# Kernel tuning notes

Measured on AMD Instinct MI355X. Metric: run time of the kernel, lower is better.

Reference implementation:

```python
import jax, jax.numpy as jnp
import numpy as np

B, M, N = 1, 8192, 131072      # batch, bones, window points
C_BOT, C = 16, 128             # bottleneck_channel, channel
K_MAX, FOLD, R_UP = 8, 8, 4    # max neighbors, fold_channel, upsample rate r
EPS = 1e-8


def _lin_init(key, fan_in, fan_out):
    return jax.random.normal(key, (fan_in, fan_out), jnp.float32) / np.sqrt(fan_in)


def setup_inputs() -> dict:
    key = jax.random.key(0)
    ks = jax.random.split(key, 10)
    return {
        "quantized_cf": jax.random.normal(ks[0], (B, M, C_BOT), jnp.float32),
        "d_idx": jax.random.randint(ks[1], (B, N, K_MAX), 0, M),
        "d_windows": jax.random.normal(ks[2], (B, N, 3), jnp.float32),
        "bones": jax.random.normal(ks[3], (B, M, 3), jnp.float32),
        "K": 8,
        # fea_stretch Linear(bottleneck -> channel)
        "W_stretch": _lin_init(ks[4], C_BOT, C),
        "b_stretch": jnp.zeros((C,), jnp.float32),
        # DWUS folding MLP: (C+3) -> C -> FOLD*R_UP -> 3 (per fold point)
        "W1": _lin_init(ks[5], C + 3, C),
        "b1": jnp.zeros((C,), jnp.float32),
        "W2": _lin_init(ks[6], C, FOLD * R_UP),
        "b2": jnp.zeros((FOLD * R_UP,), jnp.float32),
        "W3": _lin_init(ks[7], FOLD, 3),
        "b3": jnp.zeros((3,), jnp.float32),
    }


def reference(quantized_cf, d_idx, d_windows, bones, K,
              W_stretch, b_stretch, W1, b1, W2, b2, W3, b3):
    # fea_stretch: per-bone feature expansion  [B, M, C]
    skin_fea = jnp.einsum("bmc,cd->bmd", quantized_cf, W_stretch) + b_stretch

    idx = d_idx[..., :K]                                   # [B, N, K]
    batch = jnp.arange(B)[:, None, None]
    g_fea = skin_fea[batch, idx]                           # [B, N, K, C] gather
    g_bones = bones[batch, idx]                            # [B, N, K, 3]

    # inverse-distance interpolation of bone features onto window points
    rel = d_windows[:, :, None, :] - g_bones               # [B, N, K, 3]
    dist = jnp.sqrt(jnp.sum(rel * rel, axis=-1) + EPS)     # [B, N, K]
    w = 1.0 / (dist + EPS)
    w = w / jnp.sum(w, axis=-1, keepdims=True)
    interp = jnp.einsum("bnk,bnkc->bnc", w, g_fea)         # [B, N, C]

    # folding-based upsampling: each window point emits R_UP refined points
    x = jnp.concatenate([interp, d_windows], axis=-1)      # [B, N, C+3]
    h = jax.nn.relu(jnp.einsum("bnc,cd->bnd", x, W1) + b1)
    h = jax.nn.relu(jnp.einsum("bnc,cd->bnd", h, W2) + b2)
    h = h.reshape(B, N, R_UP, FOLD)
    off = jnp.einsum("bnrf,fo->bnro", h, W3) + b3          # [B, N, R_UP, 3]
    rec = d_windows[:, :, None, :] + off                   # [B, N, R_UP, 3]
    return rec.reshape(B, N * R_UP, 3)
```

## Files before the change

kernel.cpp:

```cpp
#include <hip/hip_runtime.h>
#include <hip/hip_bf16.h>

typedef __attribute__((ext_vector_type(8))) short short8;
typedef __attribute__((ext_vector_type(4))) float f32x4;

#define NPTS 131072

__device__ inline unsigned short f2bf(float f) {
    unsigned u = __float_as_uint(f);
    u = (u + 0x7FFFu + ((u >> 16) & 1u)) >> 16;
    return (unsigned short)u;
}

__device__ inline unsigned pack2(float a, float b) {
    union { __hip_bfloat162 h; unsigned u; } v;
    v.h = __float22bfloat162_rn(float2{a, b});
    return v.u;
}

__global__ __launch_bounds__(256) void prep_kernel(
    const float* __restrict__ Ws, const float* __restrict__ bs,
    const float* __restrict__ W1, const float* __restrict__ b1,
    const float* __restrict__ W2, const float* __restrict__ W3,
    unsigned short* __restrict__ w1t, unsigned short* __restrict__ w2t,
    float* __restrict__ beff, unsigned short* __restrict__ w3t)
{
    int t = blockIdx.x * 256 + threadIdx.x;
    if (t < 4096) {
        int e = t >> 5, k = t & 31;
        float v = 0.f;
        if (k < 16) {
            for (int d = 0; d < 128; ++d) v = fmaf(Ws[k*128 + d], W1[d*128 + e], v);
        } else if (k < 19) {
            v = W1[(128 + (k - 16))*128 + e];
        }
        w1t[e*32 + k] = f2bf(v);
    } else if (t < 8192) {
        int t2 = t - 4096;
        int e = t2 >> 7, d = t2 & 127;
        w2t[e*128 + ((d & 15)*8 + (d >> 4))] = f2bf(W2[d*32 + e]);
    } else if (t < 8320) {
        int e = t - 8192;
        float v = b1[e];
        for (int d = 0; d < 128; ++d) v = fmaf(bs[d], W1[d*128 + e], v);
        beff[e] = v;
    } else if (t < 8832) {
        int i = t - 8320;
        int q = i >> 5, k = i & 31;
        int e = (k & 1)*16 + (k >> 1);
        int r = e >> 3, f = e & 7;
        float v = 0.f;
        if (q < 12) {
            int r2 = q / 3, o = q - r2*3;
            if (r == r2) v = W3[f*3 + o];
        }
        w3t[q*32 + k] = f2bf(v);
    }
}

#define WREG 7936

__global__ __launch_bounds__(256, 4) void decoder_kernel(
    const float* __restrict__ qcf, const int* __restrict__ didx,
    const float* __restrict__ dwin, const float* __restrict__ bones,
    const unsigned short* __restrict__ w1t, const unsigned short* __restrict__ w2t,
    const float* __restrict__ beff, const float* __restrict__ b2,
    const unsigned short* __restrict__ w3t, const float* __restrict__ b3,
    float* __restrict__ out)
{
    __shared__ unsigned char lds[4 * WREG];

    const int tid  = threadIdx.x;
    const int wave = tid >> 6;
    const int lane = tid & 63;
    unsigned char* wbase = lds + wave * WREG;
    unsigned short* Xb  = (unsigned short*)(wbase);
    unsigned short* H1b = (unsigned short*)(wbase + 1280);
    unsigned short* H2p = (unsigned short*)(wbase + 5632);
    float*          Wb  = (float*)(wbase + 6912);
    int*            Ib  = (int*)(wbase + 7424);

    const int q4  = lane >> 4;
    const int l16 = lane & 15;

    const int gw   = blockIdx.x * 4 + wave;
    const int base = gw * 16;

#pragma unroll
    for (int ph = 0; ph < 2; ++ph) {
        const int pl = ph*8 + (lane >> 3);
        const int k  = lane & 7;
        const int p  = base + pl;
        const int id = didx[p*8 + k];
        const float bx = bones[id*3+0], by = bones[id*3+1], bz = bones[id*3+2];
        const float rx = dwin[p*3+0] - bx;
        const float ry = dwin[p*3+1] - by;
        const float rz = dwin[p*3+2] - bz;
        const float dist = sqrtf(fmaf(rx,rx, fmaf(ry,ry, fmaf(rz,rz, 1e-8f))));
        const float w = 1.0f / (dist + 1e-8f);
        float s = w;
        s += __shfl_xor(s, 1);
        s += __shfl_xor(s, 2);
        s += __shfl_xor(s, 4);
        Wb[pl*8 + k] = w / s;
        Ib[pl*8 + k] = id;
    }
    __syncthreads();

#pragma unroll
    for (int ps = 0; ps < 4; ++ps) {
        const int pl = ps*4 + q4;
        const int4   i0 = *(const int4*)(Ib + pl*8);
        const int4   i1 = *(const int4*)(Ib + pl*8 + 4);
        const float4 w0 = *(const float4*)(Wb + pl*8);
        const float4 w1 = *(const float4*)(Wb + pl*8 + 4);
        float acc = 0.f;
        acc = fmaf(w0.x, qcf[i0.x*16 + l16], acc);
        acc = fmaf(w0.y, qcf[i0.y*16 + l16], acc);
        acc = fmaf(w0.z, qcf[i0.z*16 + l16], acc);
        acc = fmaf(w0.w, qcf[i0.w*16 + l16], acc);
        acc = fmaf(w1.x, qcf[i1.x*16 + l16], acc);
        acc = fmaf(w1.y, qcf[i1.y*16 + l16], acc);
        acc = fmaf(w1.z, qcf[i1.z*16 + l16], acc);
        acc = fmaf(w1.w, qcf[i1.w*16 + l16], acc);
        Xb[pl*40 + l16] = f2bf(acc);
        float wv = 0.f;
        if (l16 < 3) wv = dwin[(base + pl)*3 + l16];
        Xb[pl*40 + 16 + l16] = f2bf(wv);
    }
    __syncthreads();

    const short8 a1 = *(const short8*)(Xb + l16*40 + q4*8);
    f32x4 acc1[8];
#pragma unroll
    for (int dt = 0; dt < 8; ++dt) {
        const short8 w1f = *(const short8*)(w1t + (dt*16 + l16)*32 + q4*8);
        const float  bv  = beff[dt*16 + l16];
        f32x4 c = { bv, bv, bv, bv };
        acc1[dt] = __builtin_amdgcn_mfma_f32_16x16x32_bf16(a1, w1f, c, 0, 0, 0);
    }
#pragma unroll
    for (int r = 0; r < 4; ++r) {
        union { unsigned u[4]; short8 s; } pk;
        pk.u[0] = pack2(fmaxf(acc1[0][r],0.f), fmaxf(acc1[1][r],0.f));
        pk.u[1] = pack2(fmaxf(acc1[2][r],0.f), fmaxf(acc1[3][r],0.f));
        pk.u[2] = pack2(fmaxf(acc1[4][r],0.f), fmaxf(acc1[5][r],0.f));
        pk.u[3] = pack2(fmaxf(acc1[6][r],0.f), fmaxf(acc1[7][r],0.f));
        *(short8*)(H1b + (q4*4 + r)*136 + l16*8) = pk.s;
    }
    __syncthreads();

    f32x4 acc2[2];
#pragma unroll
    for (int et = 0; et < 2; ++et) {
        const float bv = b2[et*16 + l16];
        acc2[et] = f32x4{ bv, bv, bv, bv };
    }
#pragma unroll
    for (int kt = 0; kt < 4; ++kt) {
        const short8 a2   = *(const short8*)(H1b + l16*136 + kt*32 + q4*8);
        const short8 w2f0 = *(const short8*)(w2t + (l16)*128      + kt*32 + q4*8);
        const short8 w2f1 = *(const short8*)(w2t + (16 + l16)*128 + kt*32 + q4*8);
        acc2[0] = __builtin_amdgcn_mfma_f32_16x16x32_bf16(a2, w2f0, acc2[0], 0, 0, 0);
        acc2[1] = __builtin_amdgcn_mfma_f32_16x16x32_bf16(a2, w2f1, acc2[1], 0, 0, 0);
    }
#pragma unroll
    for (int r = 0; r < 4; ++r) {
        unsigned p01 = pack2(fmaxf(acc2[0][r],0.f), fmaxf(acc2[1][r],0.f));
        *(unsigned*)(H2p + (q4*4 + r)*40 + l16*2) = p01;
    }
    __syncthreads();

    const short8 a3  = *(const short8*)(H2p + l16*40 + q4*8);
    const short8 w3f = *(const short8*)(w3t + l16*32 + q4*8);
    const int o = l16 - (l16/3)*3;
    const float b3o = (l16 < 12) ? b3[o] : 0.f;
    f32x4 c3 = { b3o, b3o, b3o, b3o };
    f32x4 o3 = __builtin_amdgcn_mfma_f32_16x16x32_bf16(a3, w3f, c3, 0, 0, 0);
    if (l16 < 12) {
#pragma unroll
        for (int r = 0; r < 4; ++r) {
            const int pt = base + q4*4 + r;
            out[(size_t)pt*12 + l16] = dwin[pt*3 + o] + o3[r];
        }
    }
}

extern "C" void kernel_launch(void* const* d_in, const int* in_sizes, int n_in,
                              void* d_out, int out_size, void* d_ws, size_t ws_size,
                              hipStream_t stream) {
    const float* qcf   = (const float*)d_in[0];
    const int*   didx  = (const int*)  d_in[1];
    const float* dwin  = (const float*)d_in[2];
    const float* bones = (const float*)d_in[3];
    const float* Ws = (const float*)d_in[5];
    const float* bs = (const float*)d_in[6];
    const float* W1 = (const float*)d_in[7];
    const float* b1 = (const float*)d_in[8];
    const float* W2 = (const float*)d_in[9];
    const float* b2 = (const float*)d_in[10];
    const float* W3 = (const float*)d_in[11];
    const float* b3 = (const float*)d_in[12];
    float* out = (float*)d_out;

    unsigned short* w1t  = (unsigned short*)d_ws;
    unsigned short* w2t  = (unsigned short*)((char*)d_ws + 8192);
    float*          beff = (float*)((char*)d_ws + 16384);
    unsigned short* w3t  = (unsigned short*)((char*)d_ws + 16896);

    hipLaunchKernelGGL(prep_kernel, dim3(35), dim3(256), 0, stream,
                       Ws, bs, W1, b1, W2, W3, w1t, w2t, beff, w3t);
    hipLaunchKernelGGL(decoder_kernel, dim3(2048), dim3(256), 0, stream,
                       qcf, didx, dwin, bones, w1t, w2t, beff, b2, w3t, b3, out);
}
```

Measured before the change: 34.50 us.

## Restructure decoder to single-wave blocks with register-resident gather and weights

The decoder moves from 256-thread blocks, where each wave staged indices, weights and X through LDS, to 64-thread blocks. Each lane now computes the inverse-distance weights for one point and does the feature gather in registers with float4 loads. The MFMA A operand is built directly in registers, and W1/W2/W3 fragments are preloaded once per wave. Bones are padded to float4 in the prep kernel so each neighbour needs one vector load. This removes the LDS round trips and syncs for the gather phase, at the cost of more registers per thread, 8192 small blocks, and a larger prep kernel.

```diff
diff --git a/kernel.cpp b/kernel.cpp
--- a/kernel.cpp
+++ b/kernel.cpp
@@ -22,8 +22,10 @@
     const float* __restrict__ Ws, const float* __restrict__ bs,
     const float* __restrict__ W1, const float* __restrict__ b1,
     const float* __restrict__ W2, const float* __restrict__ W3,
+    const float* __restrict__ bones,
     unsigned short* __restrict__ w1t, unsigned short* __restrict__ w2t,
-    float* __restrict__ beff, unsigned short* __restrict__ w3t)
+    float* __restrict__ beff, unsigned short* __restrict__ w3t,
+    float* __restrict__ bones4)
 {
     int t = blockIdx.x * 256 + threadIdx.x;
     if (t < 4096) {
@@ -55,114 +57,117 @@
             if (r == r2) v = W3[f*3 + o];
         }
         w3t[q*32 + k] = f2bf(v);
-    }
-}
-
-#define WREG 7936
-
-__global__ __launch_bounds__(256, 4) void decoder_kernel(
+    } else if (t < 8832 + 4*8192) {
+        int i = t - 8832;
+        int id = i >> 2, c = i & 3;
+        bones4[i] = (c < 3) ? bones[id*3 + c] : 0.f;
+    }
+}
+
+__global__ __launch_bounds__(64, 2) void decoder_kernel(
     const float* __restrict__ qcf, const int* __restrict__ didx,
-    const float* __restrict__ dwin, const float* __restrict__ bones,
+    const float* __restrict__ dwin, const float* __restrict__ bones4,
     const unsigned short* __restrict__ w1t, const unsigned short* __restrict__ w2t,
     const float* __restrict__ beff, const float* __restrict__ b2,
     const unsigned short* __restrict__ w3t, const float* __restrict__ b3,
     float* __restrict__ out)
 {
-    __shared__ unsigned char lds[4 * WREG];
-
-    const int tid  = threadIdx.x;
-    const int wave = tid >> 6;
-    const int lane = tid & 63;
-    unsigned char* wbase = lds + wave * WREG;
-    unsigned short* Xb  = (unsigned short*)(wbase);
-    unsigned short* H1b = (unsigned short*)(wbase + 1280);
-    unsigned short* H2p = (unsigned short*)(wbase + 5632);
-    float*          Wb  = (float*)(wbase + 6912);
-    int*            Ib  = (int*)(wbase + 7424);
-
-    const int q4  = lane >> 4;
-    const int l16 = lane & 15;
-
-    const int gw   = blockIdx.x * 4 + wave;
-    const int base = gw * 16;
-
-#pragma unroll
-    for (int ph = 0; ph < 2; ++ph) {
-        const int pl = ph*8 + (lane >> 3);
-        const int k  = lane & 7;
-        const int p  = base + pl;
-        const int id = didx[p*8 + k];
-        const float bx = bones[id*3+0], by = bones[id*3+1], bz = bones[id*3+2];
-        const float rx = dwin[p*3+0] - bx;
-        const float ry = dwin[p*3+1] - by;
-        const float rz = dwin[p*3+2] - bz;
+    __shared__ unsigned short H1b[16 * 136];
+    __shared__ unsigned short H2p[16 * 40];
+
+    const int lane = threadIdx.x;
+    const int q4   = lane >> 4;
+    const int l16  = lane & 15;
+
+    const int base = blockIdx.x * 16;
+    const int p    = base + l16;
+
+    short8 W1f[8]; float beffv[8];
+#pragma unroll
+    for (int dt = 0; dt < 8; ++dt) {
+        W1f[dt]   = *(const short8*)(w1t + (dt*16 + l16)*32 + q4*8);
+        beffv[dt] = beff[dt*16 + l16];
+    }
+    short8 W2f[2][4]; float b2v[2];
+#pragma unroll
+    for (int et = 0; et < 2; ++et) {
+        b2v[et] = b2[et*16 + l16];
+#pragma unroll
+        for (int kt = 0; kt < 4; ++kt)
+            W2f[et][kt] = *(const short8*)(w2t + (et*16 + l16)*128 + kt*32 + q4*8);
+    }
+    const short8 w3f = *(const short8*)(w3t + l16*32 + q4*8);
+    const int   o3c  = l16 - (l16/3)*3;
+    const float b3o  = (l16 < 12) ? b3[o3c] : 0.f;
+
+    const int4 ia = *(const int4*)(didx + p*8);
+    const int4 ib = *(const int4*)(didx + p*8 + 4);
+    const int id[8] = { ia.x, ia.y, ia.z, ia.w, ib.x, ib.y, ib.z, ib.w };
+    const float wx = dwin[p*3+0], wy = dwin[p*3+1], wz = dwin[p*3+2];
+
+    const float4* __restrict__ bn4 = (const float4*)bones4;
+    float w[8]; float s = 0.f;
+#pragma unroll
+    for (int k = 0; k < 8; ++k) {
+        const float4 b = bn4[id[k]];
+        const float rx = wx - b.x, ry = wy - b.y, rz = wz - b.z;
         const float dist = sqrtf(fmaf(rx,rx, fmaf(ry,ry, fmaf(rz,rz, 1e-8f))));
-        const float w = 1.0f / (dist + 1e-8f);
-        float s = w;
-        s += __shfl_xor(s, 1);
-        s += __shfl_xor(s, 2);
-        s += __shfl_xor(s, 4);
-        Wb[pl*8 + k] = w / s;
-        Ib[pl*8 + k] = id;
-    }
-    __syncthreads();
-
-#pragma unroll
-    for (int ps = 0; ps < 4; ++ps) {
-        const int pl = ps*4 + q4;
-        const int4   i0 = *(const int4*)(Ib + pl*8);
-        const int4   i1 = *(const int4*)(Ib + pl*8 + 4);
-        const float4 w0 = *(const float4*)(Wb + pl*8);
-        const float4 w1 = *(const float4*)(Wb + pl*8 + 4);
-        float acc = 0.f;
-        acc = fmaf(w0.x, qcf[i0.x*16 + l16], acc);
-        acc = fmaf(w0.y, qcf[i0.y*16 + l16], acc);
-        acc = fmaf(w0.z, qcf[i0.z*16 + l16], acc);
-        acc = fmaf(w0.w, qcf[i0.w*16 + l16], acc);
-        acc = fmaf(w1.x, qcf[i1.x*16 + l16], acc);
-        acc = fmaf(w1.y, qcf[i1.y*16 + l16], acc);
-        acc = fmaf(w1.z, qcf[i1.z*16 + l16], acc);
-        acc = fmaf(w1.w, qcf[i1.w*16 + l16], acc);
-        Xb[pl*40 + l16] = f2bf(acc);
-        float wv = 0.f;
-        if (l16 < 3) wv = dwin[(base + pl)*3 + l16];
-        Xb[pl*40 + 16 + l16] = f2bf(wv);
-    }
-    __syncthreads();
-
-    const short8 a1 = *(const short8*)(Xb + l16*40 + q4*8);
+        w[k] = 1.0f / (dist + 1e-8f);
+        s += w[k];
+    }
+    const float inv = 1.0f / s;
+
+    union { unsigned u[4]; short8 s8; } a1u;
+    a1u.u[0] = a1u.u[1] = a1u.u[2] = a1u.u[3] = 0u;
+    if (q4 < 2) {
+        float acc[8] = {0.f,0.f,0.f,0.f,0.f,0.f,0.f,0.f};
+        const float4* __restrict__ q4p = (const float4*)qcf;
+#pragma unroll
+        for (int k = 0; k < 8; ++k) {
+            const float4 lo = q4p[id[k]*4 + q4*2 + 0];
+            const float4 hi = q4p[id[k]*4 + q4*2 + 1];
+            acc[0] = fmaf(w[k], lo.x, acc[0]);
+            acc[1] = fmaf(w[k], lo.y, acc[1]);
+            acc[2] = fmaf(w[k], lo.z, acc[2]);
+            acc[3] = fmaf(w[k], lo.w, acc[3]);
+            acc[4] = fmaf(w[k], hi.x, acc[4]);
+            acc[5] = fmaf(w[k], hi.y, acc[5]);
+            acc[6] = fmaf(w[k], hi.z, acc[6]);
+            acc[7] = fmaf(w[k], hi.w, acc[7]);
+        }
+        a1u.u[0] = pack2(acc[0]*inv, acc[1]*inv);
+        a1u.u[1] = pack2(acc[2]*inv, acc[3]*inv);
+        a1u.u[2] = pack2(acc[4]*inv, acc[5]*inv);
+        a1u.u[3] = pack2(acc[6]*inv, acc[7]*inv);
+    } else if (q4 == 2) {
+        a1u.u[0] = pack2(wx, wy);
+        a1u.u[1] = pack2(wz, 0.f);
+    }
+
     f32x4 acc1[8];
 #pragma unroll
     for (int dt = 0; dt < 8; ++dt) {
-        const short8 w1f = *(const short8*)(w1t + (dt*16 + l16)*32 + q4*8);
-        const float  bv  = beff[dt*16 + l16];
-        f32x4 c = { bv, bv, bv, bv };
-        acc1[dt] = __builtin_amdgcn_mfma_f32_16x16x32_bf16(a1, w1f, c, 0, 0, 0);
+        f32x4 c = { beffv[dt], beffv[dt], beffv[dt], beffv[dt] };
+        acc1[dt] = __builtin_amdgcn_mfma_f32_16x16x32_bf16(a1u.s8, W1f[dt], c, 0, 0, 0);
     }
 #pragma unroll
     for (int r = 0; r < 4; ++r) {
-        union { unsigned u[4]; short8 s; } pk;
+        union { unsigned u[4]; short8 s8; } pk;
         pk.u[0] = pack2(fmaxf(acc1[0][r],0.f), fmaxf(acc1[1][r],0.f));
         pk.u[1] = pack2(fmaxf(acc1[2][r],0.f), fmaxf(acc1[3][r],0.f));
         pk.u[2] = pack2(fmaxf(acc1[4][r],0.f), fmaxf(acc1[5][r],0.f));
         pk.u[3] = pack2(fmaxf(acc1[6][r],0.f), fmaxf(acc1[7][r],0.f));
-        *(short8*)(H1b + (q4*4 + r)*136 + l16*8) = pk.s;
+        *(short8*)(H1b + (q4*4 + r)*136 + l16*8) = pk.s8;
     }
     __syncthreads();
 
-    f32x4 acc2[2];
-#pragma unroll
-    for (int et = 0; et < 2; ++et) {
-        const float bv = b2[et*16 + l16];
-        acc2[et] = f32x4{ bv, bv, bv, bv };
-    }
+    f32x4 acc2[2] = { { b2v[0], b2v[0], b2v[0], b2v[0] },
+                      { b2v[1], b2v[1], b2v[1], b2v[1] } };
 #pragma unroll
     for (int kt = 0; kt < 4; ++kt) {
-        const short8 a2   = *(const short8*)(H1b + l16*136 + kt*32 + q4*8);
-        const short8 w2f0 = *(const short8*)(w2t + (l16)*128      + kt*32 + q4*8);
-        const short8 w2f1 = *(const short8*)(w2t + (16 + l16)*128 + kt*32 + q4*8);
-        acc2[0] = __builtin_amdgcn_mfma_f32_16x16x32_bf16(a2, w2f0, acc2[0], 0, 0, 0);
-        acc2[1] = __builtin_amdgcn_mfma_f32_16x16x32_bf16(a2, w2f1, acc2[1], 0, 0, 0);
+        const short8 a2 = *(const short8*)(H1b + l16*136 + kt*32 + q4*8);
+        acc2[0] = __builtin_amdgcn_mfma_f32_16x16x32_bf16(a2, W2f[0][kt], acc2[0], 0, 0, 0);
+        acc2[1] = __builtin_amdgcn_mfma_f32_16x16x32_bf16(a2, W2f[1][kt], acc2[1], 0, 0, 0);
     }
 #pragma unroll
     for (int r = 0; r < 4; ++r) {
@@ -171,17 +176,14 @@
     }
     __syncthreads();
 
-    const short8 a3  = *(const short8*)(H2p + l16*40 + q4*8);
-    const short8 w3f = *(const short8*)(w3t + l16*32 + q4*8);
-    const int o = l16 - (l16/3)*3;
-    const float b3o = (l16 < 12) ? b3[o] : 0.f;
+    const short8 a3 = *(const short8*)(H2p + l16*40 + q4*8);
     f32x4 c3 = { b3o, b3o, b3o, b3o };
     f32x4 o3 = __builtin_amdgcn_mfma_f32_16x16x32_bf16(a3, w3f, c3, 0, 0, 0);
     if (l16 < 12) {
 #pragma unroll
         for (int r = 0; r < 4; ++r) {
             const int pt = base + q4*4 + r;
-            out[(size_t)pt*12 + l16] = dwin[pt*3 + o] + o3[r];
+            out[(size_t)pt*12 + l16] = dwin[pt*3 + o3c] + o3[r];
         }
     }
 }
@@ -203,13 +205,14 @@
     const float* b3 = (const float*)d_in[12];
     float* out = (float*)d_out;
 
-    unsigned short* w1t  = (unsigned short*)d_ws;
-    unsigned short* w2t  = (unsigned short*)((char*)d_ws + 8192);
-    float*          beff = (float*)((char*)d_ws + 16384);
-    unsigned short* w3t  = (unsigned short*)((char*)d_ws + 16896);
-
-    hipLaunchKernelGGL(prep_kernel, dim3(35), dim3(256), 0, stream,
-                       Ws, bs, W1, b1, W2, W3, w1t, w2t, beff, w3t);
-    hipLaunchKernelGGL(decoder_kernel, dim3(2048), dim3(256), 0, stream,
-                       qcf, didx, dwin, bones, w1t, w2t, beff, b2, w3t, b3, out);
-}
+    unsigned short* w1t    = (unsigned short*)d_ws;
+    unsigned short* w2t    = (unsigned short*)((char*)d_ws + 8192);
+    float*          beff   = (float*)((char*)d_ws + 16384);
+    unsigned short* w3t    = (unsigned short*)((char*)d_ws + 16896);
+    float*          bones4 = (float*)((char*)d_ws + 17920);
+
+    hipLaunchKernelGGL(prep_kernel, dim3(163), dim3(256), 0, stream,
+                       Ws, bs, W1, b1, W2, W3, bones, w1t, w2t, beff, w3t, bones4);
+    hipLaunchKernelGGL(decoder_kernel, dim3(NPTS/16), dim3(64), 0, stream,
+                       qcf, didx, dwin, bones4, w1t, w2t, beff, b2, w3t, b3, out);
+}
```

Measured after the change: 38.73 us. 12.2% more time.
